# Optimization experiments

Measured on AMD Instinct MI355X. Metric: run time of the kernel, lower is better.

The kernel has to match this reference:

```python
import jax, jax.numpy as jnp
import numpy as np

IMG = 224; P = 16; C_IN = 3; D = 768; DEPTH = 12; H = 12; HD = D // H
MLP = 4 * D; NCLS = 1000
GRID = IMG // P; NPATCH = GRID * GRID; N = NPATCH + 1
NRD = (2 * GRID - 1) * (2 * GRID - 1) + 3  # num_relative_distance


def _rel_pos_index():
    # replicates the torch buffer construction (BEiT-style)
    coords = np.stack(np.meshgrid(np.arange(GRID), np.arange(GRID), indexing='ij')).reshape(2, -1)
    rel = (coords[:, :, None] - coords[:, None, :]).transpose(1, 2, 0).astype(np.int64)
    rel[:, :, 0] += GRID - 1
    rel[:, :, 1] += GRID - 1
    rel[:, :, 0] *= 2 * GRID - 1
    idx = np.zeros((N, N), dtype=np.int64)
    idx[1:, 1:] = rel.sum(-1)
    idx[0, :] = NRD - 3
    idx[:, 0] = NRD - 2
    idx[0, 0] = NRD - 1
    return jnp.asarray(idx)

REL_IDX = _rel_pos_index()  # [N, N] int


def setup_inputs() -> dict:
    key = jax.random.key(0)
    ks = jax.random.split(key, 12)
    r = lambda k, shp: jax.random.normal(k, shp, jnp.float32) * 0.02
    return {
        'x': jax.random.normal(ks[0], (32, C_IN, IMG, IMG), jnp.float32),
        'patch_w': r(ks[1], (D, C_IN * P * P)),
        'patch_b': jnp.zeros((D,), jnp.float32),
        'cls_token': r(ks[2], (1, 1, D)),
        'pos_embed': r(ks[3], (1, N, D)),
        'norm1_s': jnp.ones((DEPTH, D), jnp.float32),
        'norm1_b': jnp.zeros((DEPTH, D), jnp.float32),
        'qkv_w': r(ks[4], (DEPTH, 3 * D, D)),
        'q_bias': jnp.zeros((DEPTH, D), jnp.float32),
        'v_bias': jnp.zeros((DEPTH, D), jnp.float32),
        'rpb_table': r(ks[5], (DEPTH, NRD, H)),
        'proj_w': r(ks[6], (DEPTH, D, D)),
        'proj_b': jnp.zeros((DEPTH, D), jnp.float32),
        'norm2_s': jnp.ones((DEPTH, D), jnp.float32),
        'norm2_b': jnp.zeros((DEPTH, D), jnp.float32),
        'fc1_w': r(ks[7], (DEPTH, MLP, D)),
        'fc1_b': jnp.zeros((DEPTH, MLP), jnp.float32),
        'fc2_w': r(ks[8], (DEPTH, D, MLP)),
        'fc2_b': jnp.zeros((DEPTH, D), jnp.float32),
        'gamma1': jnp.full((DEPTH, D), 0.1, jnp.float32),
        'gamma2': jnp.full((DEPTH, D), 0.1, jnp.float32),
        'normf_s': jnp.ones((D,), jnp.float32),
        'normf_b': jnp.zeros((D,), jnp.float32),
        'head_w': r(ks[9], (NCLS, D)),
        'head_b': jnp.zeros((NCLS,), jnp.float32),
    }


def _ln(x, s, b):
    m = jnp.mean(x, -1, keepdims=True)
    v = jnp.mean((x - m) ** 2, -1, keepdims=True)
    return (x - m) * jax.lax.rsqrt(v + 1e-5) * s + b


def reference(x, patch_w, patch_b, cls_token, pos_embed, norm1_s, norm1_b, qkv_w,
              q_bias, v_bias, rpb_table, proj_w, proj_b, norm2_s, norm2_b,
              fc1_w, fc1_b, fc2_w, fc2_b, gamma1, gamma2, normf_s, normf_b,
              head_w, head_b):
    B = x.shape[0]
    # Patch embed: stride=kernel conv == unfold + matmul
    t = x.reshape(B, C_IN, GRID, P, GRID, P).transpose(0, 2, 4, 1, 3, 5).reshape(B, NPATCH, C_IN * P * P)
    t = t @ patch_w.T + patch_b                                   # [B, 196, D]
    t = jnp.concatenate([jnp.broadcast_to(cls_token, (B, 1, D)), t], axis=1) + pos_embed
    scale = HD ** -0.5
    for i in range(DEPTH):
        h = _ln(t, norm1_s[i], norm1_b[i])
        qkv_b = jnp.concatenate([q_bias[i], jnp.zeros_like(q_bias[i]), v_bias[i]])
        qkv = (h @ qkv_w[i].T + qkv_b).reshape(B, N, 3, H, HD)
        q = qkv[:, :, 0].transpose(0, 2, 1, 3)                    # [B, H, N, HD]
        k = qkv[:, :, 1].transpose(0, 2, 1, 3)
        v = qkv[:, :, 2].transpose(0, 2, 1, 3)
        bias = rpb_table[i][REL_IDX].transpose(2, 0, 1)           # [H, N, N]
        attn = jax.nn.softmax(jnp.einsum('bhqd,bhkd->bhqk', q * scale, k) + bias[None], axis=-1)
        o = jnp.einsum('bhqk,bhkd->bhqd', attn, v).transpose(0, 2, 1, 3).reshape(B, N, D)
        t = t + gamma1[i] * (o @ proj_w[i].T + proj_b[i])
        h2 = _ln(t, norm2_s[i], norm2_b[i])
        m = jax.nn.gelu(h2 @ fc1_w[i].T + fc1_b[i], approximate=False) @ fc2_w[i].T + fc2_b[i]
        t = t + gamma2[i] * m
    t = _ln(t, normf_s, normf_b)
    return t[:, 0] @ head_w.T + head_b                            # [B, NCLS]
```

## Files before the change

kernel.cpp:

```cpp
#include <hip/hip_runtime.h>
#include <hip/hip_bf16.h>


typedef __hip_bfloat16 bf16s;
using bf16x8 = __attribute__((ext_vector_type(8))) __bf16;
using f32x4  = __attribute__((ext_vector_type(4))) float;

#define DEV static __device__ __forceinline__

DEV float b2f(bf16s x) { return __bfloat162float(x); }
DEV bf16s f2b(float x) { return __float2bfloat16(x); }

DEV void gload_lds16(const void* g, void* l) {
  __builtin_amdgcn_global_load_lds((const __attribute__((address_space(1))) void*)g,
                                   (__attribute__((address_space(3))) void*)l, 16, 0, 0);
}

constexpr int B_   = 32;
constexpr int H_   = 12;
constexpr int NTOK = 197;
constexpr int NPAD = 224;
constexpr int MVALP= 6272;
constexpr int MVAL = B_*NTOK;
constexpr int MROW = 6400;
constexpr int MLP_ = 3072;
constexpr int BH   = B_*H_;
constexpr int NRD  = 732;
constexpr int NN   = NTOK*NTOK;

constexpr size_t OFF_T   = 0;
constexpr size_t SZ_T    = (size_t)MROW*768*4;
constexpr size_t OFF_H   = OFF_T + SZ_T;
constexpr size_t SZ_H    = (size_t)MROW*768*2;
constexpr size_t OFF_Q   = OFF_H + SZ_H;
constexpr size_t SZ_QKB  = (size_t)BH*NPAD*64*2;
constexpr size_t OFF_K   = OFF_Q + SZ_QKB;
constexpr size_t OFF_VT  = OFF_K + SZ_QKB;
constexpr size_t OFF_P   = OFF_VT + SZ_QKB;
constexpr size_t SZ_P    = (size_t)MROW*MLP_*2;
constexpr size_t OFF_O   = OFF_P + SZ_P;
constexpr size_t OFF_BT  = OFF_O + SZ_H;
constexpr size_t SZ_BT   = (size_t)12*H_*NN*2;
constexpr size_t OFF_HF  = OFF_BT + SZ_BT;
constexpr size_t OFF_WB  = OFF_HF + 49152;
constexpr size_t WS_NEED = OFF_WB + (size_t)7077888*2;

constexpr size_t WB_QKV = 0;
constexpr size_t WB_PROJ= (size_t)2304*768;
constexpr size_t WB_FC1 = WB_PROJ + (size_t)768*768;
constexpr size_t WB_FC2 = WB_FC1 + (size_t)MLP_*768;

template<int MODE>
__global__ __launch_bounds__(512, 4)
void gemm8p(const bf16s* __restrict__ A, const bf16s* __restrict__ Bw,
            const int K, const int ldc,
            bf16s* __restrict__ Cb,
            const float* __restrict__ e0, const float* __restrict__ e1,
            float* __restrict__ tres,
            bf16s* __restrict__ qp, bf16s* __restrict__ kp, bf16s* __restrict__ vp)
{
  __shared__ bf16s lds[32768];
  const int tid  = threadIdx.x;
  const int lane = tid & 63;
  const int wid  = tid >> 6;
  const int wm   = wid >> 2, wn = wid & 3;

  const int ncols = gridDim.y;
  const int nwg = (int)gridDim.x * ncols;
  const int lin = (int)blockIdx.y * gridDim.x + blockIdx.x;
  const int xcd = lin & 7, pos = lin >> 3;
  const int q8 = nwg >> 3, r8 = nwg & 7;
  const int vid = (xcd < r8) ? xcd*(q8+1) + pos : r8*(q8+1) + (xcd-r8)*q8 + pos;
  constexpr int NBG = (MODE == 0) ? 6 : 8;
  const int gsz = NBG * (int)gridDim.x;
  const int g   = vid / gsz;
  const int rr  = vid - g*gsz;
  const int bm  = rr / NBG;
  const int bn  = g*NBG + (rr - bm*NBG);

  const int srow = (wid << 3) + (lane >> 3);
  const int colg = ((lane & 7) << 3) ^ (((srow >> 2) & 1) << 4);
  const bf16s* gA = A  + (size_t)(bm*128 + srow)*K + colg;
  const bf16s* gB = Bw + (size_t)(bn*128 + srow)*K + colg;
  const size_t rK64 = (size_t)64*K;

  const int r15  = lane & 15;
  const int colr = (lane >> 4) << 3;
  const int cxor = ((lane >> 2) & 1) << 4;
  const int ardA = wm*4096 + r15*64;
  const int ardB = 8192 + (wn*32 + r15)*64;

  f32x4 acc[4][2] = {};
  const int J = K >> 7;

#define STGA(h, kt, dbuf) do { \
    const bf16s* _g = gA + (size_t)(h)*rK64 + (size_t)(kt)*64; \
    gload_lds16(_g, &lds[(dbuf)*16384 + (h)*4096 + wid*512 + lane*8]); } while(0)
#define STGB(h, kt, dbuf) do { \
    const bf16s* _g = gB + (size_t)(h)*rK64 + (size_t)(kt)*64; \
    gload_lds16(_g, &lds[(dbuf)*16384 + 8192 + (h)*4096 + wid*512 + lane*8]); } while(0)

  STGB(0,0,0); STGB(1,0,0);
  STGA(0,0,0); STGA(1,0,0);
  STGB(0,1,1); STGB(1,1,1);

  bf16x8 bfr[2][2];

  for (int j = 0; j < J; ++j) {
    const bool more = (j+1 < J);
#pragma unroll
    for (int p = 0; p < 4; ++p) {
      __builtin_amdgcn_sched_barrier(0);
      if (p == 0) {
        asm volatile("s_waitcnt vmcnt(2)" ::: "memory");
      } else if (p == 2) {
        if (j+1 == J) asm volatile("s_waitcnt vmcnt(0)" ::: "memory");
        else          asm volatile("s_waitcnt vmcnt(2)" ::: "memory");
      }
      __builtin_amdgcn_sched_barrier(0);
      __builtin_amdgcn_s_barrier();
      __builtin_amdgcn_sched_barrier(0);

      if (p == 0)      { STGA(0, 2*j+1, 1); STGA(1, 2*j+1, 1); }
      else if (p == 1) { if (more) { STGB(0, 2*j+2, 0); STGB(1, 2*j+2, 0); } }
      else if (p == 2) { if (more) { STGA(0, 2*j+2, 0); STGA(1, 2*j+2, 0); } }
      else             { if (more) { STGB(0, 2*j+3, 1); STGB(1, 2*j+3, 1); } }

      const int d = (p < 2) ? 0 : 1;
      const int dbase = d*16384;
      const int q0 = (p & 1) << 1;
      if ((p & 1) == 0) {
#pragma unroll
        for (int nf=0; nf<2; nf++)
#pragma unroll
          for (int kss=0; kss<2; kss++)
            bfr[nf][kss] = *(const bf16x8*)&lds[dbase + ardB + nf*1024 + (((kss<<5) + colr) ^ cxor)];
      }
      bf16x8 a1[2][2];
#pragma unroll
      for (int qq=0; qq<2; qq++)
#pragma unroll
        for (int kss=0; kss<2; kss++)
          a1[qq][kss] = *(const bf16x8*)&lds[dbase + ardA + (q0+qq)*1024 + (((kss<<5) + colr) ^ cxor)];
      __builtin_amdgcn_s_setprio(1);
#pragma unroll
      for (int qq=0; qq<2; qq++)
#pragma unroll
        for (int nf=0; nf<2; nf++)
#pragma unroll
          for (int kss=0; kss<2; kss++)
            acc[q0+qq][nf] = __builtin_amdgcn_mfma_f32_16x16x32_bf16(a1[qq][kss], bfr[nf][kss], acc[q0+qq][nf], 0, 0, 0);
      __builtin_amdgcn_s_setprio(0);
    }
  }
#undef STGA
#undef STGB

  const int crow0 = (lane >> 4) * 4;

  if (MODE == 5) {
#pragma unroll
    for (int mf = 0; mf < 4; ++mf) {
#pragma unroll
      for (int r = 0; r < 4; ++r) {
        const int grow = bm*128 + wm*64 + mf*16 + crow0 + r;
        bf16s* crow = Cb + (size_t)grow*ldc;
#pragma unroll
        for (int nf = 0; nf < 2; ++nf) {
          const int gcol = bn*128 + wn*32 + nf*16 + r15;
          const float xx = acc[mf][nf][r] + e0[gcol];
          crow[gcol] = f2b(0.5f*xx*(1.0f + erff(xx*0.70710678118654752f)));
        }
      }
    }
    return;
  }

  if (MODE == 0 && bn >= 12) {
    float* lf = (float*)lds;
    __syncthreads();
#pragma unroll
    for (int mf = 0; mf < 4; ++mf)
#pragma unroll
      for (int nf = 0; nf < 2; ++nf)
#pragma unroll
        for (int r = 0; r < 4; ++r) {
          const int col = wn*32 + nf*16 + r15;
          const int row = wm*64 + mf*16 + crow0 + r;
          lf[col*128 + (row ^ (col & 31))] = acc[mf][nf][r];
        }
    __syncthreads();
    const int rem0 = bn*128 - 1536;
#pragma unroll
    for (int ci = 0; ci < 16; ++ci) {
      const int c = wid*16 + ci;
      const int rem = rem0 + c;
      const int hh = rem >> 6, dd = rem & 63;
      const float vb = e1[rem];
      bf16s* vrow = vp + ((size_t)hh*64 + dd)*NPAD;
#pragma unroll
      for (int hf2 = 0; hf2 < 2; ++hf2) {
        const int row = hf2*64 + lane;
        const int grow = bm*128 + row;
        if (grow < MVAL) {
          const int b2 = grow/197, ntok = grow - b2*197;
          vrow[(size_t)b2*H_*64*NPAD + ntok] = f2b(lf[c*128 + (row ^ (c & 31))] + vb);
        }
      }
    }
    return;
  }

  if (MODE == 0) {
#pragma unroll
    for (int mf = 0; mf < 4; ++mf) {
#pragma unroll
      for (int r = 0; r < 4; ++r) {
        const int grow = bm*128 + wm*64 + mf*16 + crow0 + r;
        if (grow >= MVAL) continue;
        const int bb_ = grow/197, ntok = grow - bb_*197;
#pragma unroll
        for (int nf = 0; nf < 2; ++nf) {
          const int gcol = bn*128 + wn*32 + nf*16 + r15;
          const float v = acc[mf][nf][r];
          const int rem = (gcol >= 768) ? gcol-768 : gcol;
          const int hh = rem >> 6, dd = rem & 63;
          const size_t bh = (size_t)bb_*H_ + hh;
          if (gcol < 768) qp[(bh*NPAD + ntok)*64 + dd] = f2b((v + e0[rem])*0.125f);
          else            kp[(bh*NPAD + ntok)*64 + dd] = f2b(v);
        }
      }
    }
  }
}

template<int MODE>
__global__ __launch_bounds__(256, 3)
void gemm64n(const bf16s* __restrict__ A, const bf16s* __restrict__ Bw,
             const int K, const int ldc, bf16s* __restrict__ Cb,
             const float* __restrict__ e0, const float* __restrict__ e1,
             float* __restrict__ tres)
{
  __shared__ bf16s lds[24576];
  const int tid  = threadIdx.x;
  const int lane = tid & 63;
  const int wid  = tid >> 6;
  const int wm   = wid >> 1, wn = wid & 1;

  const int ncols = gridDim.y;
  const int nwg = (int)gridDim.x * ncols;
  const int lin = (int)blockIdx.y * gridDim.x + blockIdx.x;
  const int xcd = lin & 7, pos = lin >> 3;
  const int q8 = nwg >> 3, r8 = nwg & 7;
  const int vid = (xcd < r8) ? xcd*(q8+1) + pos : r8*(q8+1) + (xcd-r8)*q8 + pos;
  const int bm = vid / ncols, bn = vid - bm*ncols;

  const int srow = tid >> 3;
  const int colg = ((tid & 7) << 3) ^ (((srow >> 2) & 1) << 4);
  const bf16s* gA = A  + (size_t)(bm*128 + srow)*K + colg;
  const bf16s* gB = Bw + (size_t)(bn*64  + srow)*K + colg;
  const size_t rK32 = (size_t)32*K;

  const int r15  = lane & 15;
  const int colr = (lane >> 4) << 3;
  const int cxor = ((lane >> 2) & 1) << 4;
  const int ardA = wm*4096 + r15*64;
  const int ardB = 8192 + (wn*32 + r15)*64;

  f32x4 acc[4][2] = {};
  const int J = K >> 7;

#define STGA2(h, kt, dbuf) do { \
    const bf16s* _g = gA + (size_t)(h)*rK32 + (size_t)(kt)*64; \
    gload_lds16(_g, &lds[(dbuf)*12288 + (h)*2048 + tid*8]); } while(0)
#define STGB2(h, kt, dbuf) do { \
    const bf16s* _g = gB + (size_t)(h)*rK32 + (size_t)(kt)*64; \
    gload_lds16(_g, &lds[(dbuf)*12288 + 8192 + (h)*2048 + tid*8]); } while(0)

  STGB2(0,0,0); STGB2(1,0,0);
  STGA2(0,0,0); STGA2(1,0,0); STGA2(2,0,0); STGA2(3,0,0);
  STGB2(0,1,1); STGB2(1,1,1);

  bf16x8 bfr[2][2];

  for (int j = 0; j < J; ++j) {
    const bool more = (j+1 < J);
#pragma unroll
    for (int p = 0; p < 4; ++p) {
      __builtin_amdgcn_sched_barrier(0);
      if (p == 0) {
        asm volatile("s_waitcnt vmcnt(2)" ::: "memory");
      } else if (p == 2) {
        if (j+1 == J) asm volatile("s_waitcnt vmcnt(0)" ::: "memory");
        else          asm volatile("s_waitcnt vmcnt(2)" ::: "memory");
      }
      __builtin_amdgcn_sched_barrier(0);
      __builtin_amdgcn_s_barrier();
      __builtin_amdgcn_sched_barrier(0);

      if (p == 0)      { STGA2(0, 2*j+1, 1); STGA2(1, 2*j+1, 1); STGA2(2, 2*j+1, 1); STGA2(3, 2*j+1, 1); }
      else if (p == 1) { if (more) { STGB2(0, 2*j+2, 0); STGB2(1, 2*j+2, 0); } }
      else if (p == 2) { if (more) { STGA2(0, 2*j+2, 0); STGA2(1, 2*j+2, 0); STGA2(2, 2*j+2, 0); STGA2(3, 2*j+2, 0); } }
      else             { if (more) { STGB2(0, 2*j+3, 1); STGB2(1, 2*j+3, 1); } }

      const int d = (p < 2) ? 0 : 1;
      const int dbase = d*12288;
      const int q0 = (p & 1) << 1;
      if ((p & 1) == 0) {
#pragma unroll
        for (int nf=0; nf<2; nf++)
#pragma unroll
          for (int kss=0; kss<2; kss++)
            bfr[nf][kss] = *(const bf16x8*)&lds[dbase + ardB + nf*1024 + (((kss<<5) + colr) ^ cxor)];
      }
      bf16x8 a1[2][2];
#pragma unroll
      for (int qq=0; qq<2; qq++)
#pragma unroll
        for (int kss=0; kss<2; kss++)
          a1[qq][kss] = *(const bf16x8*)&lds[dbase + ardA + (q0+qq)*1024 + (((kss<<5) + colr) ^ cxor)];
      __builtin_amdgcn_s_setprio(1);
#pragma unroll
      for (int qq=0; qq<2; qq++)
#pragma unroll
        for (int nf=0; nf<2; nf++)
#pragma unroll
          for (int kss=0; kss<2; kss++)
            acc[q0+qq][nf] = __builtin_amdgcn_mfma_f32_16x16x32_bf16(a1[qq][kss], bfr[nf][kss], acc[q0+qq][nf], 0, 0, 0);
      __builtin_amdgcn_s_setprio(0);
    }
  }
#undef STGA2
#undef STGB2

  const int crow0 = (lane >> 4) * 4;
#pragma unroll
  for (int mf = 0; mf < 4; ++mf) {
#pragma unroll
    for (int r = 0; r < 4; ++r) {
      const int grow = bm*128 + wm*64 + mf*16 + crow0 + r;
      if (MODE == 3) {
        bf16s* crow = Cb + (size_t)grow*ldc;
#pragma unroll
        for (int nf = 0; nf < 2; ++nf) {
          const int gcol = bn*64 + wn*32 + nf*16 + r15;
          const float xx = acc[mf][nf][r] + e0[gcol];
          crow[gcol] = f2b(0.5f*xx*(1.0f + erff(xx*0.70710678118654752f)));
        }
      } else {
        float* trow = tres + (size_t)grow*768;
#pragma unroll
        for (int nf = 0; nf < 2; ++nf) {
          const int gcol = bn*64 + wn*32 + nf*16 + r15;
          trow[gcol] += e1[gcol]*(acc[mf][nf][r] + e0[gcol]);
        }
      }
    }
  }
}

__global__ __launch_bounds__(256, 5)
void gemm64p(const bf16s* __restrict__ A, const bf16s* __restrict__ Bw,
             int K,
             const float* __restrict__ e0, const float* __restrict__ e1,
             float* __restrict__ tres)
{
  __shared__ bf16s As[2][64*32];
  __shared__ bf16s Bs[2][128*32];
  const int tid  = threadIdx.x;
  const int lane = tid & 63;
  const int wave = tid >> 6;

  const int ncols = gridDim.y;
  const int nwg = (int)gridDim.x * ncols;
  const int lin = (int)blockIdx.y * gridDim.x + blockIdx.x;
  const int xcd = lin & 7, pos = lin >> 3;
  const int q8 = nwg >> 3, r8 = nwg & 7;
  const int vid = (xcd < r8) ? xcd*(q8+1) + pos : r8*(q8+1) + (xcd-r8)*q8 + pos;
  const int bm = vid / ncols, bn = vid - bm*ncols;

  f32x4 acc[2][4] = {};

  const int sr4  = lane >> 2;
  const int scol = ((lane&3) ^ (sr4&3))*8;
  const bf16s* gA = A  + (size_t)(bm*64  + wave*16 + sr4)*K + scol;
  const bf16s* gB = Bw + (size_t)(bn*128 + wave*32 + sr4)*K + scol;
  const size_t b16 = (size_t)16*K;
  const int dA  = wave*512  + lane*8;
  const int dB0 = wave*1024 + lane*8, dB1 = dB0 + 512;

  const int fr  = lane & 15;
  const int rdk = (((lane>>4) ^ (lane&3)))*8;
  const int wr = wave >> 1, wc = wave & 1;
  const int abase = (wr*32 + fr)*32 + rdk;
  const int bbase = (wc*64 + fr)*32 + rdk;

  const int nk = K >> 5;
  gload_lds16(gA,       &As[0][dA]);
  gload_lds16(gB,       &Bs[0][dB0]);
  gload_lds16(gB + b16, &Bs[0][dB1]);

  int cur = 0;
  for (int kt = 0; kt < nk; ++kt) {
    __syncthreads();
    if (kt + 1 < nk) {
      const bf16s* ga = gA + (size_t)(kt+1)*32;
      const bf16s* gb = gB + (size_t)(kt+1)*32;
      gload_lds16(ga,       &As[cur^1][dA]);
      gload_lds16(gb,       &Bs[cur^1][dB0]);
      gload_lds16(gb + b16, &Bs[cur^1][dB1]);
    }
    bf16x8 af[2], bfr[4];
    af[0] = *(const bf16x8*)&As[cur][abase];
    af[1] = *(const bf16x8*)&As[cur][abase + 512];
#pragma unroll
    for (int n2=0;n2<4;n2++) bfr[n2] = *(const bf16x8*)&Bs[cur][bbase + n2*512];
#pragma unroll
    for (int m=0;m<2;m++)
#pragma unroll
      for (int n2=0;n2<4;n2++)
        acc[m][n2] = __builtin_amdgcn_mfma_f32_16x16x32_bf16(af[m], bfr[n2], acc[m][n2], 0, 0, 0);
    cur ^= 1;
  }

  const int crow0 = (lane>>4)*4;
#pragma unroll
  for (int m=0;m<2;m++) {
#pragma unroll
    for (int r=0;r<4;r++) {
      const int grow = bm*64 + wr*32 + m*16 + crow0 + r;
      if (grow >= MVALP) continue;
      const int bb_ = grow/196, p = grow - bb_*196;
      float* trow = tres + ((size_t)bb_*197 + 1 + p)*768;
      const float* prow = e1 + (size_t)(1+p)*768;
#pragma unroll
      for (int n2=0;n2<4;n2++) {
        const int gcol = bn*128 + wc*64 + n2*16 + fr;
        trow[gcol] = acc[m][n2][r] + e0[gcol] + prow[gcol];
      }
    }
  }
}

__global__ __launch_bounds__(256)
void f2b_k(const float* __restrict__ src, bf16s* __restrict__ dst, int n4)
{
  int id = blockIdx.x*256 + threadIdx.x;
  if (id >= n4) return;
  const float4 v = ((const float4*)src)[id];
  union { bf16s b[4]; uint2 u; } uu;
  uu.b[0] = f2b(v.x); uu.b[1] = f2b(v.y); uu.b[2] = f2b(v.z); uu.b[3] = f2b(v.w);
  ((uint2*)dst)[id] = uu.u;
}

__global__ __launch_bounds__(256)
void prep_k(const float* __restrict__ tin, const float* __restrict__ s,
            const float* __restrict__ b, bf16s* __restrict__ outp,
            const float* __restrict__ qw, const float* __restrict__ pw,
            const float* __restrict__ f1, const float* __restrict__ f2,
            bf16s* __restrict__ wb)
{
  const int tid = threadIdx.x;
  if (blockIdx.x < MVAL) {
    const int r = blockIdx.x;
    const float* xr = tin + (size_t)r*768;
    float v0 = xr[tid], v1 = xr[tid+256], v2 = xr[tid+512];
    float sum = v0+v1+v2;
#pragma unroll
    for (int off=32; off>=1; off>>=1) sum += __shfl_xor(sum, off, 64);
    __shared__ float red[8];
    const int wv = tid>>6, ln = tid&63;
    if (ln==0) red[wv] = sum;
    __syncthreads();
    const float mean = (red[0]+red[1]+red[2]+red[3]) * (1.0f/768.0f);
    const float d0=v0-mean, d1=v1-mean, d2=v2-mean;
    float sq = d0*d0 + d1*d1 + d2*d2;
#pragma unroll
    for (int off=32; off>=1; off>>=1) sq += __shfl_xor(sq, off, 64);
    if (ln==0) red[4+wv] = sq;
    __syncthreads();
    const float rs = rsqrtf((red[4]+red[5]+red[6]+red[7])*(1.0f/768.0f) + 1e-5f);
    bf16s* orow = outp + (size_t)r*768;
    orow[tid]     = f2b(d0*rs*s[tid]     + b[tid]);
    orow[tid+256] = f2b(d1*rs*s[tid+256] + b[tid+256]);
    orow[tid+512] = f2b(d2*rs*s[tid+512] + b[tid+512]);
  } else {
    int id = (blockIdx.x - MVAL)*256 + tid;
    const float* src; size_t dst; int loc;
    if (id < 442368)           { src = qw; loc = id;          dst = WB_QKV; }
    else if (id < 589824)      { src = pw; loc = id-442368;   dst = WB_PROJ; }
    else if (id < 1179648)     { src = f1; loc = id-589824;   dst = WB_FC1; }
    else                       { src = f2; loc = id-1179648;  dst = WB_FC2; }
    const float4 v = ((const float4*)src)[loc];
    union { bf16s bb[4]; uint2 u; } uu;
    uu.bb[0] = f2b(v.x); uu.bb[1] = f2b(v.y); uu.bb[2] = f2b(v.z); uu.bb[3] = f2b(v.w);
    ((uint2*)(wb + dst))[loc] = uu.u;
  }
}

__global__ __launch_bounds__(256)
void bias_all_k(const float* __restrict__ rpb, bf16s* __restrict__ biasT)
{
  int id = blockIdx.x*256 + threadIdx.x;
  if (id >= 12*H_*NN) return;
  const int l   = id / (H_*NN);
  const int r2  = id - l*(H_*NN);
  const int hh  = r2 / NN;
  const int rem = r2 - hh*NN;
  const int i = rem / 197, j = rem - i*197;
  int v;
  if (i==0 && j==0)      v = NRD-1;
  else if (i==0)         v = NRD-3;
  else if (j==0)         v = NRD-2;
  else {
    const int p = i-1, q = j-1;
    v = (p/14 - q/14 + 13)*27 + (p%14 - q%14 + 13);
  }
  biasT[id] = f2b(rpb[(size_t)l*NRD*H_ + v*H_ + hh]);
}

__global__ __launch_bounds__(256)
void im2col_k(const float* __restrict__ x, bf16s* __restrict__ pat)
{
  int id = blockIdx.x*256 + threadIdx.x;
  if (id >= MVALP*768) return;
  int col = id % 768;  int row = id / 768;
  int b = row / 196, p = row % 196;
  int gy = p / 14, gx = p % 14;
  int c = col >> 8, rem = col & 255, py = rem >> 4, px = rem & 15;
  pat[id] = f2b(x[ ((size_t)(b*3 + c)*224 + gy*16 + py)*224 + gx*16 + px ]);
}

__global__ __launch_bounds__(256)
void clspos_k(const float* __restrict__ cls, const float* __restrict__ pos, float* __restrict__ t)
{
  int id = blockIdx.x*256 + threadIdx.x;
  int d = id % 768, b = id / 768;
  t[(size_t)b*197*768 + d] = cls[d] + pos[d];
}

__global__ __launch_bounds__(256)
void ln_k(const float* __restrict__ tin, const float* __restrict__ s,
          const float* __restrict__ b, bf16s* __restrict__ outp, int instride)
{
  const int r = blockIdx.x, tid = threadIdx.x;
  const float* xr = tin + (size_t)r*instride;
  float v0 = xr[tid], v1 = xr[tid+256], v2 = xr[tid+512];
  float sum = v0+v1+v2;
#pragma unroll
  for (int off=32; off>=1; off>>=1) sum += __shfl_xor(sum, off, 64);
  __shared__ float red[8];
  const int wv = tid>>6, ln = tid&63;
  if (ln==0) red[wv] = sum;
  __syncthreads();
  const float mean = (red[0]+red[1]+red[2]+red[3]) * (1.0f/768.0f);
  const float d0=v0-mean, d1=v1-mean, d2=v2-mean;
  float sq = d0*d0 + d1*d1 + d2*d2;
#pragma unroll
  for (int off=32; off>=1; off>>=1) sq += __shfl_xor(sq, off, 64);
  if (ln==0) red[4+wv] = sq;
  __syncthreads();
  const float rs = rsqrtf((red[4]+red[5]+red[6]+red[7])*(1.0f/768.0f) + 1e-5f);
  bf16s* orow = outp + (size_t)r*768;
  orow[tid]     = f2b(d0*rs*s[tid]     + b[tid]);
  orow[tid+256] = f2b(d1*rs*s[tid+256] + b[tid+256]);
  orow[tid+512] = f2b(d2*rs*s[tid+512] + b[tid+512]);
}

__global__ __launch_bounds__(64)
void attn_fused(const bf16s* __restrict__ q, const bf16s* __restrict__ k,
                const bf16s* __restrict__ vT, const bf16s* __restrict__ biasT,
                bf16s* __restrict__ o)
{
  __shared__ bf16s Pl[32][232];
  const int gid = blockIdx.x;
  const int qt = gid % 7, bh = gid / 7;
  const int b = bh / H_, hh = bh % H_;
  const int lane = threadIdx.x;
  const int fr = lane & 15, fk = (lane>>4)*8;
  const bf16s* qp = q + (size_t)bh*NPAD*64;
  const bf16s* kp = k + (size_t)bh*NPAD*64;
  bf16x8 a[2][2];
#pragma unroll
  for (int m=0;m<2;m++)
#pragma unroll
    for (int kk=0;kk<2;kk++)
      a[m][kk] = *(const bf16x8*)&qp[(qt*32 + m*16 + fr)*64 + kk*32 + fk];

  f32x4 acc[2][14] = {};
#pragma unroll
  for (int nt=0; nt<14; nt++) {
    bf16x8 bb0 = *(const bf16x8*)&kp[(nt*16 + fr)*64 + fk];
    bf16x8 bb1 = *(const bf16x8*)&kp[(nt*16 + fr)*64 + 32 + fk];
    acc[0][nt] = __builtin_amdgcn_mfma_f32_16x16x32_bf16(a[0][0], bb0, acc[0][nt], 0,0,0);
    acc[0][nt] = __builtin_amdgcn_mfma_f32_16x16x32_bf16(a[0][1], bb1, acc[0][nt], 0,0,0);
    acc[1][nt] = __builtin_amdgcn_mfma_f32_16x16x32_bf16(a[1][0], bb0, acc[1][nt], 0,0,0);
    acc[1][nt] = __builtin_amdgcn_mfma_f32_16x16x32_bf16(a[1][1], bb1, acc[1][nt], 0,0,0);
  }

  const bf16s* bT = biasT + (size_t)hh*NN;
#pragma unroll
  for (int m=0;m<2;m++) {
#pragma unroll
    for (int r2=0;r2<4;r2++) {
      const int lrow = m*16 + (lane>>4)*4 + r2;
      const int row = qt*32 + lrow;
      if (row < NTOK) {
        const bf16s* br = bT + (size_t)row*197;
        float s[14]; float mx = -3.0e38f;
#pragma unroll
        for (int nt=0; nt<14; nt++) {
          const int col = nt*16 + fr;
          float v = acc[m][nt][r2] + ((col < NTOK) ? b2f(br[col]) : 0.0f);
          s[nt] = v;
          if (col < NTOK) mx = fmaxf(mx, v);
        }
        mx = fmaxf(mx, __shfl_xor(mx, 1, 64));
        mx = fmaxf(mx, __shfl_xor(mx, 2, 64));
        mx = fmaxf(mx, __shfl_xor(mx, 4, 64));
        mx = fmaxf(mx, __shfl_xor(mx, 8, 64));
        float sum = 0.f;
#pragma unroll
        for (int nt=0; nt<14; nt++) {
          const int col = nt*16 + fr;
          float p = (col < NTOK) ? __expf(s[nt]-mx) : 0.0f;
          s[nt] = p; sum += p;
        }
        sum += __shfl_xor(sum, 1, 64);
        sum += __shfl_xor(sum, 2, 64);
        sum += __shfl_xor(sum, 4, 64);
        sum += __shfl_xor(sum, 8, 64);
        const float inv = 1.0f / sum;
#pragma unroll
        for (int nt=0; nt<14; nt++)
          Pl[lrow][nt*16 + fr] = f2b(s[nt]*inv);
      } else {
#pragma unroll
        for (int nt=0; nt<14; nt++)
          Pl[lrow][nt*16 + fr] = f2b(0.0f);
      }
    }
  }

  __syncthreads();

  const bf16s* Vp = vT + (size_t)bh*64*NPAD;
  f32x4 pacc[2][4] = {};
  for (int kt=0; kt<7; kt++) {
    bf16x8 a0 = *(const bf16x8*)&Pl[fr][kt*32 + fk];
    bf16x8 a1 = *(const bf16x8*)&Pl[16 + fr][kt*32 + fk];
#pragma unroll
    for (int nf=0;nf<4;nf++) {
      bf16x8 bb = *(const bf16x8*)&Vp[(size_t)(nf*16 + fr)*NPAD + kt*32 + fk];
      pacc[0][nf] = __builtin_amdgcn_mfma_f32_16x16x32_bf16(a0, bb, pacc[0][nf], 0,0,0);
      pacc[1][nf] = __builtin_amdgcn_mfma_f32_16x16x32_bf16(a1, bb, pacc[1][nf], 0,0,0);
    }
  }

  __syncthreads();
#pragma unroll
  for (int m=0;m<2;m++)
#pragma unroll
    for (int nf=0;nf<4;nf++)
#pragma unroll
      for (int r2=0;r2<4;r2++)
        Pl[m*16 + (lane>>4)*4 + r2][nf*16 + fr] = f2b(pacc[m][nf][r2]);
  __syncthreads();
  bf16s* obase = o + ((size_t)b*NTOK + qt*32)*768 + hh*64;
#pragma unroll
  for (int it=0; it<8; ++it) {
    const int id = it*64 + lane;
    const int row = id >> 4, c4 = (id & 15)*4;
    if (qt*32 + row < NTOK) {
      union { bf16s bb[4]; uint2 u; } uu;
      uu.bb[0]=Pl[row][c4]; uu.bb[1]=Pl[row][c4+1]; uu.bb[2]=Pl[row][c4+2]; uu.bb[3]=Pl[row][c4+3];
      *(uint2*)&obase[(size_t)row*768 + c4] = uu.u;
    }
  }
}

__global__ __launch_bounds__(256)
void head_k(const bf16s* __restrict__ hf, const float* __restrict__ hw,
            const float* __restrict__ hb, float* __restrict__ outp)
{
  const int b = blockIdx.y;
  const int n = blockIdx.x*256 + threadIdx.x;
  __shared__ float xs[768];
  for (int i=threadIdx.x; i<768; i+=256) xs[i] = b2f(hf[b*768+i]);
  __syncthreads();
  if (n < 1000) {
    const float* wr = hw + (size_t)n*768;
    float acc2 = hb[n];
    for (int k2=0;k2<768;k2++) acc2 += xs[k2]*wr[k2];
    outp[b*1000 + n] = acc2;
  }
}

extern "C" void kernel_launch(void* const* d_in, const int* in_sizes, int n_in,
                              void* d_out, int out_size, void* d_ws, size_t ws_size,
                              hipStream_t stream)
{
  const float* x       = (const float*)d_in[0];
  const float* patch_w = (const float*)d_in[1];
  const float* patch_b = (const float*)d_in[2];
  const float* cls_tok = (const float*)d_in[3];
  const float* pos_emb = (const float*)d_in[4];
  const float* norm1_s = (const float*)d_in[5];
  const float* norm1_b = (const float*)d_in[6];
  const float* qkv_w   = (const float*)d_in[7];
  const float* q_bias  = (const float*)d_in[8];
  const float* v_bias  = (const float*)d_in[9];
  const float* rpb     = (const float*)d_in[10];
  const float* proj_w  = (const float*)d_in[11];
  const float* proj_b  = (const float*)d_in[12];
  const float* norm2_s = (const float*)d_in[13];
  const float* norm2_b = (const float*)d_in[14];
  const float* fc1_w   = (const float*)d_in[15];
  const float* fc1_b   = (const float*)d_in[16];
  const float* fc2_w   = (const float*)d_in[17];
  const float* fc2_b   = (const float*)d_in[18];
  const float* gamma1  = (const float*)d_in[19];
  const float* gamma2  = (const float*)d_in[20];
  const float* normf_s = (const float*)d_in[21];
  const float* normf_b = (const float*)d_in[22];
  const float* head_w  = (const float*)d_in[23];
  const float* head_b  = (const float*)d_in[24];
  float* out = (float*)d_out;

  char* w = (char*)d_ws;
  float* t    = (float*)(w + OFF_T);
  bf16s* h    = (bf16s*)(w + OFF_H);
  bf16s* qb   = (bf16s*)(w + OFF_Q);
  bf16s* kb   = (bf16s*)(w + OFF_K);
  bf16s* vT   = (bf16s*)(w + OFF_VT);
  bf16s* m1   = (bf16s*)(w + OFF_P);
  bf16s* pat  = (bf16s*)(w + OFF_P);
  bf16s* o    = (bf16s*)(w + OFF_O);
  bf16s* biasT= (bf16s*)(w + OFF_BT);
  bf16s* hf   = (bf16s*)(w + OFF_HF);
  bf16s* wb   = (bf16s*)(w + OFF_WB);
  (void)ws_size; (void)in_sizes; (void)n_in; (void)out_size; (void)WS_NEED;

  hipMemsetAsync(h  + (size_t)MVAL*768,  0, (size_t)(MROW-MVAL)*768*2,  stream);
  hipMemsetAsync(o  + (size_t)MVAL*768,  0, (size_t)(MROW-MVAL)*768*2,  stream);
  hipMemsetAsync(m1 + (size_t)MVAL*MLP_, 0, (size_t)(MROW-MVAL)*MLP_*2, stream);
  hipMemsetAsync(qb, 0, SZ_QKB, stream);
  hipMemsetAsync(kb, 0, SZ_QKB, stream);
  hipMemsetAsync(vT, 0, SZ_QKB, stream);

  bias_all_k<<<(12*H_*NN + 255)/256, 256, 0, stream>>>(rpb, biasT);
  im2col_k<<<(MVALP*768)/256, 256, 0, stream>>>(x, pat);
  clspos_k<<<96, 256, 0, stream>>>(cls_tok, pos_emb, t);
  f2b_k<<<(768*768/4)/256, 256, 0, stream>>>(patch_w, wb, 768*768/4);
  gemm64p<<<dim3(98,6), 256, 0, stream>>>(pat, wb, 768, patch_b, pos_emb, t);

  for (int l = 0; l < 12; ++l) {
    prep_k<<<MVAL + 6912, 256, 0, stream>>>(t, norm1_s + l*768, norm1_b + l*768, h,
                                            qkv_w + (size_t)l*2304*768, proj_w + (size_t)l*768*768,
                                            fc1_w + (size_t)l*MLP_*768, fc2_w + (size_t)l*768*MLP_, wb);
    gemm8p<0><<<dim3(50,18), 512, 0, stream>>>(h, wb + WB_QKV, 768, 2304, nullptr,
                                               q_bias + l*768, v_bias + l*768, nullptr,
                                               qb, kb, vT);
    attn_fused<<<BH*7, 64, 0, stream>>>(qb, kb, vT, biasT + (size_t)l*H_*NN, o);
    gemm64n<2><<<dim3(50,12), 256, 0, stream>>>(o, wb + WB_PROJ, 768, 0, nullptr,
                                                proj_b + l*768, gamma1 + l*768, t);
    ln_k<<<MVAL, 256, 0, stream>>>(t, norm2_s + l*768, norm2_b + l*768, h, 768);
    gemm8p<5><<<dim3(50,24), 512, 0, stream>>>(h, wb + WB_FC1, 768, MLP_, m1,
                                               fc1_b + l*MLP_, nullptr, nullptr,
                                               nullptr, nullptr, nullptr);
    gemm64n<4><<<dim3(50,12), 256, 0, stream>>>(m1, wb + WB_FC2, 3072, 0, nullptr,
                                                fc2_b + l*768, gamma2 + l*768, t);
  }

  ln_k<<<32, 256, 0, stream>>>(t, normf_s, normf_b, hf, 197*768);
  head_k<<<dim3(4,32), 256, 0, stream>>>(hf, head_w, head_b, out);
}
```

Measured before the change: 2.822 ms.

## Split-K the FC2 GEMM on the 128x128 kernel with atomic residual accumulation

The FC2 projection (K=3072) moves from the gemm64n kernel onto the larger 128x128-tile gemm8p kernel, with K split into four slices of 768. This gives 1200 workgroups instead of 600 for better occupancy. Each slice atomically adds its gamma2-scaled partial result into the fp32 residual stream, and only the first slice adds the bias. The cost is fp32 atomic traffic on the residual, and the summation order is no longer deterministic.

```diff
diff --git a/kernel.cpp b/kernel.cpp
--- a/kernel.cpp
+++ b/kernel.cpp
@@ -71,18 +71,28 @@
   const int xcd = lin & 7, pos = lin >> 3;
   const int q8 = nwg >> 3, r8 = nwg & 7;
   const int vid = (xcd < r8) ? xcd*(q8+1) + pos : r8*(q8+1) + (xcd-r8)*q8 + pos;
-  constexpr int NBG = (MODE == 0) ? 6 : 8;
-  const int gsz = NBG * (int)gridDim.x;
-  const int g   = vid / gsz;
-  const int rr  = vid - g*gsz;
-  const int bm  = rr / NBG;
-  const int bn  = g*NBG + (rr - bm*NBG);
-
+
+  int bm, bn, koff = 0, ksl = 0;
+  if (MODE == 6) {
+    ksl = vid / 300;
+    const int rem = vid - ksl*300;
+    bm = rem / 6; bn = rem - bm*6;
+    koff = ksl * 768;
+  } else {
+    constexpr int NBG = (MODE == 0) ? 6 : 8;
+    const int gsz = NBG * (int)gridDim.x;
+    const int g   = vid / gsz;
+    const int rr  = vid - g*gsz;
+    bm  = rr / NBG;
+    bn  = g*NBG + (rr - bm*NBG);
+  }
+
+  const int ldk = (MODE == 6) ? ldc : K;
   const int srow = (wid << 3) + (lane >> 3);
   const int colg = ((lane & 7) << 3) ^ (((srow >> 2) & 1) << 4);
-  const bf16s* gA = A  + (size_t)(bm*128 + srow)*K + colg;
-  const bf16s* gB = Bw + (size_t)(bn*128 + srow)*K + colg;
-  const size_t rK64 = (size_t)64*K;
+  const bf16s* gA = A  + (size_t)(bm*128 + srow)*ldk + koff + colg;
+  const bf16s* gB = Bw + (size_t)(bn*128 + srow)*ldk + koff + colg;
+  const size_t rK64 = (size_t)64*ldk;
 
   const int r15  = lane & 15;
   const int colr = (lane >> 4) << 3;
@@ -157,6 +167,24 @@
 #undef STGB
 
   const int crow0 = (lane >> 4) * 4;
+
+  if (MODE == 6) {
+#pragma unroll
+    for (int mf = 0; mf < 4; ++mf) {
+#pragma unroll
+      for (int r = 0; r < 4; ++r) {
+        const int grow = bm*128 + wm*64 + mf*16 + crow0 + r;
+        float* trow = tres + (size_t)grow*768;
+#pragma unroll
+        for (int nf = 0; nf < 2; ++nf) {
+          const int gcol = bn*128 + wn*32 + nf*16 + r15;
+          const float add = e1[gcol]*(acc[mf][nf][r] + ((ksl == 0) ? e0[gcol] : 0.0f));
+          unsafeAtomicAdd(&trow[gcol], add);
+        }
+      }
+    }
+    return;
+  }
 
   if (MODE == 5) {
 #pragma unroll
@@ -768,8 +796,9 @@
     gemm8p<5><<<dim3(50,24), 512, 0, stream>>>(h, wb + WB_FC1, 768, MLP_, m1,
                                                fc1_b + l*MLP_, nullptr, nullptr,
                                                nullptr, nullptr, nullptr);
-    gemm64n<4><<<dim3(50,12), 256, 0, stream>>>(m1, wb + WB_FC2, 3072, 0, nullptr,
-                                                fc2_b + l*768, gamma2 + l*768, t);
+    gemm8p<6><<<dim3(50,24), 512, 0, stream>>>(m1, wb + WB_FC2, 768, MLP_, nullptr,
+                                               fc2_b + l*768, gamma2 + l*768, t,
+                                               nullptr, nullptr, nullptr);
   }
 
   ln_k<<<32, 256, 0, stream>>>(t, normf_s, normf_b, hf, 197*768);
```

Measured after the change: 3.272 ms. +15.9%, slower.
